# Kernel tuning notes

Hardware: AMD Instinct MI355X
Metric: run time of the kernel (lower is better)

Reference implementation:

```python
import jax, jax.numpy as jnp
import numpy as np

IN_FEATURES = 4096
OUT_FEATURES = 14336
BATCH = 2
SEQ = 2048
INT4_ZERO = 8  # stored uint-style int4 values in [0,16); signed value = q - 8


def setup_inputs() -> dict:
    key = jax.random.key(0)
    k_x, k_w, k_s, k_b = jax.random.split(key, 4)
    x = jax.random.normal(k_x, (BATCH, SEQ, IN_FEATURES), dtype=jnp.float32)
    weight_q = jax.random.randint(k_w, (OUT_FEATURES, IN_FEATURES), 0, 16, dtype=jnp.int32)
    weight_scale = jax.random.uniform(k_s, (OUT_FEATURES, 1), dtype=jnp.float32)
    bias = jax.random.normal(k_b, (OUT_FEATURES,), dtype=jnp.float32)
    return {"x": x, "weight_q": weight_q, "weight_scale": weight_scale, "bias": bias}


def reference(x, weight_q, weight_scale, bias):
    orig_shape = x.shape
    x2d = x.reshape(-1, orig_shape[-1])  # [T, in]
    # fused int4 dequant + matmul + bias: w = (q - zero) * per-row scale
    w = (weight_q.astype(x.dtype) - INT4_ZERO) * weight_scale  # [out, in]
    y2d = jnp.einsum('ti,oi->to', x2d, w) + bias  # [T, out]
    return y2d.reshape(*orig_shape[:-1], w.shape[0])
```

## Files before the change

### kernel.cpp

```cpp
#include <hip/hip_runtime.h>


#define AS1 __attribute__((address_space(1)))
#define AS3 __attribute__((address_space(3)))

typedef __attribute__((ext_vector_type(8))) short short8;
typedef __attribute__((ext_vector_type(4))) float f32x4;

static constexpr int IN_F   = 4096;
static constexpr int OUT_F  = 14336;
static constexpr int TOKENS = 4096;


__device__ __forceinline__ unsigned short bf16_rne(float f) {
    unsigned int u = __float_as_uint(f);
    u += 0x7fffu + ((u >> 16) & 1u);
    return (unsigned short)(u >> 16);
}

__global__ void convert_kernel(const int4* __restrict__ q, ushort4* __restrict__ wb,
                               const float4* __restrict__ x, ushort4* __restrict__ xb) {
    constexpr size_t NW = (size_t)OUT_F * IN_F / 4;
    constexpr size_t NX = (size_t)TOKENS * IN_F / 4;
    const size_t stride = (size_t)gridDim.x * blockDim.x;
    for (size_t i = (size_t)blockIdx.x * blockDim.x + threadIdx.x; i < NW + NX;
         i += stride) {
        if (i < NW) {
            int4 v = q[i];
            ushort4 r;
            r.x = (unsigned short)(__float_as_uint((float)(v.x - 8)) >> 16);
            r.y = (unsigned short)(__float_as_uint((float)(v.y - 8)) >> 16);
            r.z = (unsigned short)(__float_as_uint((float)(v.z - 8)) >> 16);
            r.w = (unsigned short)(__float_as_uint((float)(v.w - 8)) >> 16);
            wb[i] = r;
        } else {
            size_t j = i - NW;
            float4 v = x[j];
            ushort4 r;
            r.x = bf16_rne(v.x); r.y = bf16_rne(v.y);
            r.z = bf16_rne(v.z); r.w = bf16_rne(v.w);
            xb[j] = r;
        }
    }
}


#define STAGE(T_, Q_, MATP_)                                                               \
    do {                                                                                   \
        const unsigned short* g_ = ((Q_) < 2 ? gA : gB) + ((Q_) & 1) * (size_t)(128 * K)   \
                                   + (size_t)(T_) * BK;                                    \
        unsigned short* l_ = (MATP_) + ((Q_) & 1) * HS + tid * 8;                          \
        __builtin_amdgcn_global_load_lds((const AS1 void*)g_, (AS3 void*)l_, 16, 0, 0);    \
        __builtin_amdgcn_global_load_lds((const AS1 void*)(g_ + (size_t)64 * K),           \
                                         (AS3 void*)(l_ + 4096), 16, 0, 0);                \
    } while (0)

#define BAR()                                                                              \
    do {                                                                                   \
        asm volatile("" ::: "memory");                                                     \
        __builtin_amdgcn_s_barrier();                                                      \
        asm volatile("" ::: "memory");                                                     \
    } while (0)

#define MFMA_QUAD(M0_, N0_)                                                                \
    __builtin_amdgcn_s_setprio(1);                                                         \
    _Pragma("unroll") for (int s_ = 0; s_ < 2; ++s_)                                       \
        _Pragma("unroll") for (int m_ = 0; m_ < 4; ++m_)                                   \
            _Pragma("unroll") for (int n_ = 0; n_ < 2; ++n_)                               \
                acc[(M0_) + m_][(N0_) + n_] = __builtin_amdgcn_mfma_f32_16x16x32_bf16(     \
                    af[(M0_) + m_][s_], bf[(N0_) + n_][s_],                                \
                    acc[(M0_) + m_][(N0_) + n_], 0, 0, 0);                                 \
    __builtin_amdgcn_s_setprio(0);

#define KTILE(T_, TA_, TB_, NXA_, NXB_)                                                    \
    do {                                                                                   \
             \
        _Pragma("unroll") for (int m_ = 0; m_ < 4; ++m_) {                                 \
            af[m_][0] = *(const short8*)((TA_) + aOff  + m_ * 1024);                       \
            af[m_][1] = *(const short8*)((TA_) + aOffB + m_ * 1024);                       \
        }                                                                                  \
        _Pragma("unroll") for (int n_ = 0; n_ < 2; ++n_) {                                 \
            bf[n_][0] = *(const short8*)((TB_) + bOff  + n_ * 1024);                       \
            bf[n_][1] = *(const short8*)((TB_) + bOffB + n_ * 1024);                       \
        }                                                                                  \
        if ((T_) + 1 < NT) STAGE((T_) + 1, 2, NXB_);                                       \
        BAR();                                                                             \
        MFMA_QUAD(0, 0)                                                                    \
        BAR();                                                                             \
                      \
        _Pragma("unroll") for (int m_ = 0; m_ < 4; ++m_) {                                 \
            af[4 + m_][0] = *(const short8*)((TA_) + aOff  + (4 + m_) * 1024);             \
            af[4 + m_][1] = *(const short8*)((TA_) + aOffB + (4 + m_) * 1024);             \
        }                                                                                  \
        _Pragma("unroll") for (int n_ = 0; n_ < 2; ++n_) {                                 \
            bf[2 + n_][0] = *(const short8*)((TB_) + bOff  + (2 + n_) * 1024);             \
            bf[2 + n_][1] = *(const short8*)((TB_) + bOffB + (2 + n_) * 1024);             \
        }                                                                                  \
        if ((T_) + 1 < NT) STAGE((T_) + 1, 3, NXB_);                                       \
        BAR();                                                                             \
        MFMA_QUAD(4, 0)                                                                    \
        BAR();                                                                             \
                                        \
        if ((T_) + 2 < NT) STAGE((T_) + 2, 0, NXA_);                                       \
        BAR();                                                                             \
        MFMA_QUAD(0, 2)                                                                    \
        BAR();                                                                             \
                         \
        if ((T_) + 2 < NT) STAGE((T_) + 2, 1, NXA_);                                       \
        BAR();                                                                             \
        MFMA_QUAD(4, 2)                                                                    \
        if ((T_) + 2 < NT) {                                                               \
            asm volatile("s_waitcnt vmcnt(4)" ::: "memory");                               \
        } else {                                                                           \
            asm volatile("s_waitcnt vmcnt(0)" ::: "memory");                               \
        }                                                                                  \
        BAR();                                                                             \
    } while (0)

__global__ __launch_bounds__(512, 2)
void gemm256_kernel(const unsigned short* __restrict__ A,
                    const unsigned short* __restrict__ B,
                    const float* __restrict__ scale,
                    const float* __restrict__ bias,
                    float* __restrict__ C) {
    constexpr int K  = IN_F;
    constexpr int N  = OUT_F;
    constexpr int BK = 64;
    constexpr int NT = K / BK;
    constexpr int TS = 256 * BK;
    constexpr int HS = TS / 2;

    __shared__ unsigned short sm[2][2][TS];

    const int tid  = threadIdx.x;
    const int lane = tid & 63;
    const int wave = tid >> 6;
    const int l16  = lane & 15;
    const int lq   = lane >> 4;
    const int wr   = wave >> 2;
    const int wc   = wave & 3;

    const int bid   = blockIdx.y * 56 + blockIdx.x;
    const int swz   = (bid & 7) * 112 + (bid >> 3);
    const int nBase = (swz % 56) * 256;
    const int mBase = (swz / 56) * 256;

    const int srow = tid >> 3;
    const int scol = ((tid ^ (tid >> 3)) & 7) * 8;
    const unsigned short* gA = A + (size_t)(mBase + srow) * K + scol;
    const unsigned short* gB = B + (size_t)(nBase + srow) * K + scol;

    const int klane = lq ^ (l16 & 7);
    const int aOff  = (wr * 128 + l16) * 64 + klane * 8;
    const int bOff  = (wc * 64  + l16) * 64 + klane * 8;
    const int aOffB = aOff ^ 32;
    const int bOffB = bOff ^ 32;

    f32x4  acc[8][4] = {};
    short8 af[8][2];
    short8 bf[4][2];

    unsigned short* smA0 = &sm[0][0][0];
    unsigned short* smB0 = &sm[0][1][0];
    unsigned short* smA1 = &sm[1][0][0];
    unsigned short* smB1 = &sm[1][1][0];

    STAGE(0, 0, smA0); STAGE(0, 1, smA0); STAGE(0, 2, smB0); STAGE(0, 3, smB0);
    STAGE(1, 0, smA1); STAGE(1, 1, smA1);
    asm volatile("s_waitcnt vmcnt(4)" ::: "memory");
    BAR();

    for (int t = 0; t < NT; t += 2) {
        KTILE(t,     smA0, smB0, smA0, smB1);
        KTILE(t + 1, smA1, smB1, smA1, smB0);
    }

#pragma unroll
    for (int n = 0; n < 4; ++n) {
        const int col  = nBase + wc * 64 + n * 16 + l16;
        const float s  = scale[col];
        const float bb = bias[col];
#pragma unroll
        for (int m = 0; m < 8; ++m) {
            const int row0 = mBase + wr * 128 + m * 16 + lq * 4;
            float* cp = C + (size_t)row0 * N + col;
#pragma unroll
            for (int r = 0; r < 4; ++r)
                cp[(size_t)r * N] = acc[m][n][r] * s + bb;
        }
    }
}


extern "C" void kernel_launch(void* const* d_in, const int* in_sizes, int n_in,
                              void* d_out, int out_size, void* d_ws, size_t ws_size,
                              hipStream_t stream) {
    const float* x      = (const float*)d_in[0];
    const int*   wq     = (const int*)d_in[1];
    const float* wscale = (const float*)d_in[2];
    const float* wbias  = (const float*)d_in[3];
    float* out = (float*)d_out;

    unsigned short* wbf = (unsigned short*)d_ws;
    unsigned short* xbf = wbf + (size_t)OUT_F * IN_F;

    convert_kernel<<<2048, 256, 0, stream>>>((const int4*)wq, (ushort4*)wbf,
                                             (const float4*)x, (ushort4*)xbf);

    gemm256_kernel<<<dim3(56, 16), 512, 0, stream>>>(xbf, wbf, wscale, wbias, out);
}
```

Before: 869.4 us.

## Software-pipeline LDS fragment reads across k-tiles to overlap with MFMA

Restructures the k-tile loop so that A and B register fragments for the next quarter or the next tile are read from shared memory before the barrier and MFMA block that precede their use, instead of right before it. The first A/B fragments of the next tile are prefetched at the end of the current tile, and the prologue is split with extra waitcnt and barrier steps. The aim is to hide LDS read latency behind matrix ops. In exchange the buffer roles and barrier ordering change, which risks read/write races on shared memory and adds register pressure.

Result: no change. 863.8 us (-0.7%).

```diff
diff --git a/kernel.cpp b/kernel.cpp
--- a/kernel.cpp
+++ b/kernel.cpp
@@ -72,41 +72,40 @@
                     acc[(M0_) + m_][(N0_) + n_], 0, 0, 0);                                 \
     __builtin_amdgcn_s_setprio(0);
 
-#define KTILE(T_, TA_, TB_, NXA_, NXB_)                                                    \
+#define RD_A(LO_, SRCP_)                                                                   \
+    _Pragma("unroll") for (int m_ = 0; m_ < 4; ++m_) {                                     \
+        af[(LO_) + m_][0] = *(const short8*)((SRCP_) + aOff  + ((LO_) + m_) * 1024);       \
+        af[(LO_) + m_][1] = *(const short8*)((SRCP_) + aOffB + ((LO_) + m_) * 1024);       \
+    }
+#define RD_B(LO_, SRCP_)                                                                   \
+    _Pragma("unroll") for (int n_ = 0; n_ < 2; ++n_) {                                     \
+        bf[(LO_) + n_][0] = *(const short8*)((SRCP_) + bOff  + ((LO_) + n_) * 1024);       \
+        bf[(LO_) + n_][1] = *(const short8*)((SRCP_) + bOffB + ((LO_) + n_) * 1024);       \
+    }
+
+#define KTILE(T_, TA_, TB_, NA_, NB_)                                                      \
     do {                                                                                   \
-             \
-        _Pragma("unroll") for (int m_ = 0; m_ < 4; ++m_) {                                 \
-            af[m_][0] = *(const short8*)((TA_) + aOff  + m_ * 1024);                       \
-            af[m_][1] = *(const short8*)((TA_) + aOffB + m_ * 1024);                       \
-        }                                                                                  \
-        _Pragma("unroll") for (int n_ = 0; n_ < 2; ++n_) {                                 \
-            bf[n_][0] = *(const short8*)((TB_) + bOff  + n_ * 1024);                       \
-            bf[n_][1] = *(const short8*)((TB_) + bOffB + n_ * 1024);                       \
-        }                                                                                  \
-        if ((T_) + 1 < NT) STAGE((T_) + 1, 2, NXB_);                                       \
+                        \
+        if ((T_) + 1 < NT) STAGE((T_) + 1, 2, NB_);                                        \
+        RD_A(4, TA_)                                                                       \
         BAR();                                                                             \
         MFMA_QUAD(0, 0)                                                                    \
         BAR();                                                                             \
-                      \
-        _Pragma("unroll") for (int m_ = 0; m_ < 4; ++m_) {                                 \
-            af[4 + m_][0] = *(const short8*)((TA_) + aOff  + (4 + m_) * 1024);             \
-            af[4 + m_][1] = *(const short8*)((TA_) + aOffB + (4 + m_) * 1024);             \
-        }                                                                                  \
-        _Pragma("unroll") for (int n_ = 0; n_ < 2; ++n_) {                                 \
-            bf[2 + n_][0] = *(const short8*)((TB_) + bOff  + (2 + n_) * 1024);             \
-            bf[2 + n_][1] = *(const short8*)((TB_) + bOffB + (2 + n_) * 1024);             \
-        }                                                                                  \
-        if ((T_) + 1 < NT) STAGE((T_) + 1, 3, NXB_);                                       \
+                        \
+        if ((T_) + 1 < NT) STAGE((T_) + 1, 3, NB_);                                        \
+        RD_B(2, TB_)                                                                       \
         BAR();                                                                             \
         MFMA_QUAD(4, 0)                                                                    \
         BAR();                                                                             \
-                                        \
-        if ((T_) + 2 < NT) STAGE((T_) + 2, 0, NXA_);                                       \
+                          \
+        asm volatile("s_waitcnt vmcnt(4)" ::: "memory");                                   \
+        if ((T_) + 2 < NT) STAGE((T_) + 2, 0, TA_);                                        \
         BAR();                                                                             \
         MFMA_QUAD(0, 2)                                                                    \
         BAR();                                                                             \
-                         \
-        if ((T_) + 2 < NT) STAGE((T_) + 2, 1, NXA_);                                       \
+        if ((T_) + 1 < NT) { RD_A(0, NA_) }                                                \
+                          \
+        if ((T_) + 2 < NT) STAGE((T_) + 2, 1, TA_);                                        \
         BAR();                                                                             \
         MFMA_QUAD(4, 2)                                                                    \
         if ((T_) + 2 < NT) {                                                               \
@@ -115,6 +114,7 @@
             asm volatile("s_waitcnt vmcnt(0)" ::: "memory");                               \
         }                                                                                  \
         BAR();                                                                             \
+        if ((T_) + 1 < NT) { RD_B(0, NB_) }                                                \
     } while (0)
 
 __global__ __launch_bounds__(512, 2)
@@ -167,12 +167,16 @@
 
     STAGE(0, 0, smA0); STAGE(0, 1, smA0); STAGE(0, 2, smB0); STAGE(0, 3, smB0);
     STAGE(1, 0, smA1); STAGE(1, 1, smA1);
+    asm volatile("s_waitcnt vmcnt(8)" ::: "memory");
+    BAR();
+    RD_A(0, smA0)
     asm volatile("s_waitcnt vmcnt(4)" ::: "memory");
     BAR();
+    RD_B(0, smB0)
 
     for (int t = 0; t < NT; t += 2) {
-        KTILE(t,     smA0, smB0, smA0, smB1);
-        KTILE(t + 1, smA1, smB1, smA1, smB0);
+        KTILE(t,     smA0, smB0, smA1, smB1);
+        KTILE(t + 1, smA1, smB1, smA0, smB0);
     }
 
 #pragma unroll
```
